# Optimization experiments

Hardware: AMD Instinct MI355X
Metric: run time of the kernel (lower is better)

Reference implementation:

```python
import jax, jax.numpy as jnp
import numpy as np


def _l2norm(x, eps=1e-12):
    # F.normalize(p=2, dim=-1): x / max(||x||_2, eps)
    n = jnp.linalg.norm(x, axis=-1, keepdims=True)
    return x / jnp.maximum(n, eps)


def _dwconv3x3(x, w):
    # depthwise 3x3 conv, padding=1, no bias. x: [B,C,H,W], w: [C,1,3,3]
    return jax.lax.conv_general_dilated(
        x, w, window_strides=(1, 1), padding='SAME',
        feature_group_count=x.shape[1],
        dimension_numbers=('NCHW', 'OIHW', 'NCHW'))


def setup_inputs() -> dict:
    key = jax.random.key(0)
    ks = jax.random.split(key, 10)
    B, H, W, C = 2, 256, 256, 64
    heads, dh, dim_out = 8, 64, 64
    hd = heads * dh  # 512
    s = 0.02
    return {
        'x_in': jax.random.normal(ks[0], (B, H, W, C), jnp.float32),
        'Wq': jax.random.normal(ks[1], (C, hd), jnp.float32) * s,
        'Wk': jax.random.normal(ks[2], (C, hd), jnp.float32) * s,
        'Wv': jax.random.normal(ks[3], (C, hd), jnp.float32) * s,
        'rescale': jnp.ones((heads, 1, 1), jnp.float32),
        'Wproj': jax.random.normal(ks[4], (hd, dim_out), jnp.float32) * s,
        'bproj': jnp.zeros((dim_out,), jnp.float32),
        'Wc1d': jax.random.normal(ks[5], (hd, dim_out), jnp.float32) * s,
        'bc1d': jnp.zeros((dim_out,), jnp.float32),
        'Wpe1': jax.random.normal(ks[6], (dim_out, 1, 3, 3), jnp.float32) * s,
        'Wpe2': jax.random.normal(ks[7], (dim_out, 1, 3, 3), jnp.float32) * s,
    }


def reference(x_in, Wq, Wk, Wv, rescale, Wproj, bproj, Wc1d, bc1d, Wpe1, Wpe2):
    b, h, w, c = x_in.shape
    heads = rescale.shape[0]
    hd = Wq.shape[1]
    dh = hd // heads
    dim_out = Wproj.shape[1]
    ds = 2

    # AvgPool2d(2,2) on channels-last input
    xp = x_in.reshape(b, h // ds, ds, w // ds, ds, c).mean(axis=(2, 4))
    n_ds = (h // ds) * (w // ds)
    xd = xp.reshape(b, n_ds, c)

    # q,k from downsampled tokens; v from full-res tokens
    q = (xd @ Wq).reshape(b, n_ds, heads, dh).transpose(0, 2, 3, 1)   # [b,heads,dh,n_ds]
    k = (xd @ Wk).reshape(b, n_ds, heads, dh).transpose(0, 2, 3, 1)   # [b,heads,dh,n_ds]
    v_inp = x_in.reshape(b, h * w, c) @ Wv                             # [b,n,hd]
    v = v_inp.reshape(b, h * w, heads, dh).transpose(0, 2, 3, 1)       # [b,heads,dh,n]

    q = _l2norm(q)
    k = _l2norm(k)

    # channel (transposed) attention: [b,heads,dh,dh]
    attn = jnp.einsum('bhin,bhjn->bhij', k, q) * rescale
    attn = jax.nn.softmax(attn, axis=-1)

    xa = jnp.einsum('bhij,bhjn->bhin', attn, v)                        # [b,heads,dh,n]
    xa = xa.transpose(0, 3, 1, 2).reshape(b, h * w, hd)                # [b,n,hd]
    out_c = (xa @ Wproj + bproj).reshape(b, h, w, dim_out)

    # positional branch: 1x1 conv (pointwise) then two depthwise 3x3 convs with GELU
    p = v_inp @ Wc1d + bc1d                                            # [b,n,dim_out]
    p = p.reshape(b, h, w, dim_out).transpose(0, 3, 1, 2)              # [b,dim_out,h,w]
    p = _dwconv3x3(p, Wpe1)
    p = jax.nn.gelu(p, approximate=False)
    p = _dwconv3x3(p, Wpe2)
    out_p = p.transpose(0, 2, 3, 1)                                    # [b,h,w,dim_out]

    return out_c + out_p
```

## Files before the change

kernel.cpp:

```cpp
#include <hip/hip_runtime.h>
#include <math.h>


typedef unsigned short u16;
typedef unsigned int u32;
typedef __attribute__((ext_vector_type(8))) short short8;
typedef __attribute__((ext_vector_type(4))) float f32x4;

__device__ __forceinline__ float bf2f(u16 h) { return __uint_as_float(((u32)h) << 16); }
__device__ __forceinline__ u16 f2bf(float f) {
    u32 u = __float_as_uint(f);
    return (u16)((u + 0x7fffu + ((u >> 16) & 1u)) >> 16);
}
__device__ __forceinline__ float rbf(float f) { return bf2f(f2bf(f)); }
__device__ __forceinline__ u32 pk2(float lo, float hi) {
    return (u32)f2bf(lo) | ((u32)f2bf(hi) << 16);
}
__device__ __forceinline__ void unpack8(uint4 v, float* f) {
    u32 a[4] = {v.x, v.y, v.z, v.w};
#pragma unroll
    for (int i = 0; i < 4; ++i) {
        f[2 * i]     = __uint_as_float(a[i] << 16);
        f[2 * i + 1] = __uint_as_float(a[i] & 0xffff0000u);
    }
}
__device__ __forceinline__ float gelu_exact(float v) {
    return 0.5f * v * (1.f + erff(v * 0.70710678118654752f));
}

__global__ __launch_bounds__(256) void k_front(
    const float* __restrict__ x,
    const float* __restrict__ wq_f, const float* __restrict__ wk_f,
    const float* __restrict__ wv_f, const float* __restrict__ rs_f,
    const float* __restrict__ wp_f, const float* __restrict__ bp_f,
    const float* __restrict__ wc_f, const float* __restrict__ bc_f,
    const float* __restrict__ p1_f, const float* __restrict__ p2_f,
    u32* __restrict__ wb32, float* __restrict__ Wpos,
    u16* __restrict__ xb, float* __restrict__ partials) {
    __shared__ float xvs[64 * 68];
    int blk = blockIdx.x;
    int t = threadIdx.x;
    if (blk < 323) {
        u32 pid = (u32)blk * 256u + t;
        if (pid < 82564u) {
            const float* src; u32 p;
            if      (pid < 16384u) { src = wq_f; p = pid; }
            else if (pid < 32768u) { src = wk_f; p = pid - 16384u; }
            else if (pid < 49152u) { src = wv_f; p = pid - 32768u; }
            else if (pid < 49156u) { src = rs_f; p = pid - 49152u; }
            else if (pid < 65540u) { src = wp_f; p = pid - 49156u; }
            else if (pid < 65572u) { src = bp_f; p = pid - 65540u; }
            else if (pid < 81956u) { src = wc_f; p = pid - 65572u; }
            else if (pid < 81988u) { src = bc_f; p = pid - 81956u; }
            else if (pid < 82276u) { src = p1_f; p = pid - 81988u; }
            else                   { src = p2_f; p = pid - 82276u; }
            wb32[pid] = (u32)f2bf(src[2 * p]) | ((u32)f2bf(src[2 * p + 1]) << 16);
        }
    } else if (blk < 387) {
        int c = blk - 323;
        int o = t & 63, ch = t >> 6;
        const float* wvr = wv_f + c * 512 + ch * 128;
        const float* wcr = wc_f + (size_t)(ch * 128) * 64 + o;
        float s = 0.f;
        for (int kk = 0; kk < 128; ++kk)
            s += rbf(wvr[kk]) * rbf(wcr[(size_t)kk * 64]);
        xvs[ch * 64 + o] = s;
        __syncthreads();
        if (t < 64)
            Wpos[c * 64 + t] = (xvs[t] + xvs[64 + t]) + (xvs[128 + t] + xvs[192 + t]);
    } else {
        int gb = blk - 387;
        int b = gb >> 8, sub = gb & 255;
        int py = sub >> 1, half = sub & 1;
        const size_t rowbase = (size_t)(b * 256 + 2 * py) * 16384 + (size_t)half * 8192;
#pragma unroll
        for (int i2 = 0; i2 < 4; ++i2) {
            int u = t + 256 * i2;
            int P = u >> 4, cq = u & 15;
            size_t o0 = rowbase + (size_t)(2 * P) * 64 + cq * 4;
            float4 a0 = *(const float4*)(x + o0);
            float4 a1 = *(const float4*)(x + o0 + 64);
            float4 a2 = *(const float4*)(x + o0 + 16384);
            float4 a3 = *(const float4*)(x + o0 + 16384 + 64);
            *(uint2*)(xb + o0)              = make_uint2(pk2(a0.x, a0.y), pk2(a0.z, a0.w));
            *(uint2*)(xb + o0 + 64)         = make_uint2(pk2(a1.x, a1.y), pk2(a1.z, a1.w));
            *(uint2*)(xb + o0 + 16384)      = make_uint2(pk2(a2.x, a2.y), pk2(a2.z, a2.w));
            *(uint2*)(xb + o0 + 16384 + 64) = make_uint2(pk2(a3.x, a3.y), pk2(a3.z, a3.w));
            float4 s;
            s.x = 0.25f * (a0.x + a1.x + a2.x + a3.x);
            s.y = 0.25f * (a0.y + a1.y + a2.y + a3.y);
            s.z = 0.25f * (a0.z + a1.z + a2.z + a3.z);
            s.w = 0.25f * (a0.w + a1.w + a2.w + a3.w);
            *(float4*)(&xvs[P * 68 + cq * 4]) = s;
        }
        __syncthreads();
        int r0 = (t >> 4) << 2, c0 = (t & 15) << 2;
        float acc[4][4] = {{0.f}};
        for (int P = 0; P < 64; ++P) {
            float4 av = *(const float4*)(&xvs[P * 68 + r0]);
            float4 bv = *(const float4*)(&xvs[P * 68 + c0]);
            float ar[4] = {av.x, av.y, av.z, av.w};
            float br[4] = {bv.x, bv.y, bv.z, bv.w};
#pragma unroll
            for (int i = 0; i < 4; ++i)
#pragma unroll
                for (int j = 0; j < 4; ++j)
                    acc[i][j] += ar[i] * br[j];
        }
        float* outp = partials + (size_t)gb * 4096;
#pragma unroll
        for (int i = 0; i < 4; ++i)
            *(float4*)(&outp[(r0 + i) * 64 + c0]) =
                make_float4(acc[i][0], acc[i][1], acc[i][2], acc[i][3]);
    }
}

__global__ __launch_bounds__(256) void k_mid1(
    const float* __restrict__ partials, float* __restrict__ G4, float* __restrict__ Weff,
    const u16* __restrict__ xb, const float* __restrict__ Wpos,
    const u16* __restrict__ bc1d, u16* __restrict__ pbuf) {
    __shared__ u16 sm[128 * 72];
    int blk = blockIdx.x;
    int t = threadIdx.x;
    if (blk < 128) {
        int gid = blk * 256 + t;
        int e = gid & 4095, ch = (gid >> 12) & 3, b = gid >> 14;
        const float* p0 = partials + ((size_t)(b * 256 + ch * 64)) * 4096 + e;
        float s = 0.f;
        for (int p = 0; p < 64; ++p)
            s += p0[(size_t)p * 4096];
        G4[gid] = s;
        if (gid < 8192) Weff[gid] = 0.f;
        return;
    }
    int pb = blk - 128;
    int lane = t & 63, wv = t >> 6;
    int col = lane & 15, quad = lane >> 4;

    short8 bf[2][4];
#pragma unroll
    for (int kh = 0; kh < 2; ++kh)
#pragma unroll
        for (int nt = 0; nt < 4; ++nt) {
            short8 v;
#pragma unroll
            for (int j = 0; j < 8; ++j)
                v[j] = (short)f2bf(Wpos[(kh * 32 + quad * 8 + j) * 64 + nt * 16 + col]);
            bf[kh][nt] = v;
        }
    float bias[4];
#pragma unroll
    for (int nt = 0; nt < 4; ++nt) bias[nt] = bf2f(bc1d[nt * 16 + col]);

    size_t base = (size_t)pb * 128;
#pragma unroll
    for (int g = 0; g < 2; ++g) {
        int P0 = wv * 32 + g * 16;
        const short8* ap = (const short8*)(xb + (base + P0 + col) * 64);
        short8 a0 = ap[quad];
        short8 a1 = ap[4 + quad];
#pragma unroll
        for (int nt = 0; nt < 4; ++nt) {
            f32x4 acc = {0.f, 0.f, 0.f, 0.f};
            acc = __builtin_amdgcn_mfma_f32_16x16x32_bf16(a0, bf[0][nt], acc, 0, 0, 0);
            acc = __builtin_amdgcn_mfma_f32_16x16x32_bf16(a1, bf[1][nt], acc, 0, 0, 0);
#pragma unroll
            for (int r = 0; r < 4; ++r)
                sm[(P0 + quad * 4 + r) * 72 + nt * 16 + col] = f2bf(acc[r] + bias[nt]);
        }
    }
    __syncthreads();
#pragma unroll
    for (int k = 0; k < 4; ++k) {
        int linear = k * 256 + t;
        int px = linear >> 3, oct = linear & 7;
        uint4 v = *(const uint4*)(&sm[px * 72 + oct * 8]);
        *(uint4*)(pbuf + (base + px) * 64 + oct * 8) = v;
    }
}

__global__ __launch_bounds__(256) void k_mid2(
    const u16* __restrict__ wkb, const u16* __restrict__ wqb,
    const u16* __restrict__ wpb, const u16* __restrict__ wvb,
    const u16* __restrict__ rsb,
    const float* __restrict__ G4, float* __restrict__ Weff,
    const u16* __restrict__ pbuf, const u16* __restrict__ wpe1, u16* __restrict__ tbuf) {
    __shared__ __align__(16) char shm[53248];
    int blk = blockIdx.x, t = threadIdx.x;
    if (blk < 16) {
        float* Ts   = (float*)shm;
        float* Ps   = (float*)(shm + 17408);
        float* Gs   = (float*)(shm + 34816);
        u16*   Wpjs = (u16*)(shm + 34816);
        u16*   Wvs  = (u16*)(shm + 34816 + 9216);
        float* attns = Ps;
        float* Pls   = Ts;
        int b = blk >> 3, h = blk & 7;
        int c = t >> 2, jq = t & 3, j0 = jq * 16;
        {
            int base = t * 16;
            int row = base >> 6, col = base & 63;
            const float* Gb = G4 + (size_t)b * 16384;
#pragma unroll
            for (int q = 0; q < 4; ++q) {
                float4 g0 = *(const float4*)(&Gb[base + 4 * q]);
                float4 g1 = *(const float4*)(&Gb[4096 + base + 4 * q]);
                float4 g2 = *(const float4*)(&Gb[8192 + base + 4 * q]);
                float4 g3 = *(const float4*)(&Gb[12288 + base + 4 * q]);
                *(float4*)(&Gs[row * 68 + col + 4 * q]) = make_float4(
                    (g0.x + g1.x) + (g2.x + g3.x), (g0.y + g1.y) + (g2.y + g3.y),
                    (g0.z + g1.z) + (g2.z + g3.z), (g0.w + g1.w) + (g2.w + g3.w));
            }
        }
        __syncthreads();
        float Tr[16];
        {
#pragma unroll
            for (int jj = 0; jj < 16; ++jj) Tr[jj] = 0.f;
            for (int k = 0; k < 64; ++k) {
                short8 w0 = *(const short8*)(&wkb[k * 512 + h * 64 + j0]);
                short8 w1 = *(const short8*)(&wkb[k * 512 + h * 64 + j0 + 8]);
                float g = Gs[c * 68 + k];
#pragma unroll
                for (int jj = 0; jj < 8; ++jj) {
                    Tr[jj]     += g * bf2f((u16)w0[jj]);
                    Tr[8 + jj] += g * bf2f((u16)w1[jj]);
                }
            }
            short8 wc0 = *(const short8*)(&wkb[c * 512 + h * 64 + j0]);
            short8 wc1 = *(const short8*)(&wkb[c * 512 + h * 64 + j0 + 8]);
#pragma unroll
            for (int jj = 0; jj < 8; ++jj) {
                Ps[c * 68 + j0 + jj]     = bf2f((u16)wc0[jj]) * Tr[jj];
                Ps[c * 68 + j0 + 8 + jj] = bf2f((u16)wc1[jj]) * Tr[8 + jj];
            }
        }
        __syncthreads();
        if (t < 64) {
            float s = 0.f;
            for (int cc = 0; cc < 64; ++cc) s += Ps[cc * 68 + t];
            Ts[t * 68 + 64] = fmaxf(sqrtf(fmaxf(s, 0.f)), 1e-12f);
        }
        {
#pragma unroll
            for (int jj = 0; jj < 16; ++jj) Tr[jj] = 0.f;
            for (int k = 0; k < 64; ++k) {
                short8 w0 = *(const short8*)(&wqb[k * 512 + h * 64 + j0]);
                short8 w1 = *(const short8*)(&wqb[k * 512 + h * 64 + j0 + 8]);
                float g = Gs[c * 68 + k];
#pragma unroll
                for (int jj = 0; jj < 8; ++jj) {
                    Tr[jj]     += g * bf2f((u16)w0[jj]);
                    Tr[8 + jj] += g * bf2f((u16)w1[jj]);
                }
            }
#pragma unroll
            for (int q = 0; q < 4; ++q)
                *(float4*)(&Ts[c * 68 + j0 + 4 * q]) =
                    make_float4(Tr[4 * q], Tr[4 * q + 1], Tr[4 * q + 2], Tr[4 * q + 3]);
        }
        __syncthreads();
        {
            short8 wc0 = *(const short8*)(&wqb[c * 512 + h * 64 + j0]);
            short8 wc1 = *(const short8*)(&wqb[c * 512 + h * 64 + j0 + 8]);
#pragma unroll
            for (int jj = 0; jj < 8; ++jj) {
                Ps[c * 68 + j0 + jj]     = bf2f((u16)wc0[jj]) * Tr[jj];
                Ps[c * 68 + j0 + 8 + jj] = bf2f((u16)wc1[jj]) * Tr[8 + jj];
            }
            *(short8*)(&Wpjs[c * 72 + j0])     = *(const short8*)(&wpb[(h * 64 + c) * 64 + j0]);
            *(short8*)(&Wpjs[c * 72 + j0 + 8]) = *(const short8*)(&wpb[(h * 64 + c) * 64 + j0 + 8]);
        }
        __syncthreads();
        if (t < 64) {
            float s = 0.f;
            for (int cc = 0; cc < 64; ++cc) s += Ps[cc * 68 + t];
            Ts[t * 68 + 65] = fmaxf(sqrtf(fmaxf(s, 0.f)), 1e-12f);
        }
        __syncthreads();
        {
            int i = t >> 2;
            float L[16];
#pragma unroll
            for (int jj = 0; jj < 16; ++jj) L[jj] = 0.f;
            for (int c2 = 0; c2 < 64; ++c2) {
                float wk = bf2f(wkb[c2 * 512 + h * 64 + i]);
#pragma unroll
                for (int q = 0; q < 4; ++q) {
                    float4 tv = *(const float4*)(&Ts[c2 * 68 + j0 + 4 * q]);
                    L[4 * q + 0] += wk * tv.x;
                    L[4 * q + 1] += wk * tv.y;
                    L[4 * q + 2] += wk * tv.z;
                    L[4 * q + 3] += wk * tv.w;
                }
            }
            float rs = bf2f(rsb[h]);
            float nki = Ts[i * 68 + 64];
            float nqv[16];
#pragma unroll
            for (int jj = 0; jj < 16; ++jj) nqv[jj] = Ts[(j0 + jj) * 68 + 65];
            float m = -1e30f;
#pragma unroll
            for (int jj = 0; jj < 16; ++jj) {
                L[jj] = L[jj] * rs / (nki * nqv[jj]);
                m = fmaxf(m, L[jj]);
            }
            m = fmaxf(m, __shfl_xor(m, 1));
            m = fmaxf(m, __shfl_xor(m, 2));
            float s = 0.f;
#pragma unroll
            for (int jj = 0; jj < 16; ++jj) {
                L[jj] = __expf(L[jj] - m);
                s += L[jj];
            }
            s += __shfl_xor(s, 1);
            s += __shfl_xor(s, 2);
            float inv = 1.f / s;
#pragma unroll
            for (int q = 0; q < 4; ++q)
                *(float4*)(&attns[i * 68 + j0 + 4 * q]) =
                    make_float4(L[4 * q] * inv, L[4 * q + 1] * inv,
                                L[4 * q + 2] * inv, L[4 * q + 3] * inv);
        }
        __syncthreads();
        {
            *(short8*)(&Wvs[c * 72 + j0])     = *(const short8*)(&wvb[c * 512 + h * 64 + j0]);
            *(short8*)(&Wvs[c * 72 + j0 + 8]) = *(const short8*)(&wvb[c * 512 + h * 64 + j0 + 8]);
            int j = t >> 2, oq = t & 3;
            float Pl[16];
#pragma unroll
            for (int jj = 0; jj < 16; ++jj) Pl[jj] = 0.f;
            for (int i2 = 0; i2 < 64; ++i2) {
                float a = attns[i2 * 68 + j];
                short8 w0 = *(const short8*)(&Wpjs[i2 * 72 + oq * 16]);
                short8 w1 = *(const short8*)(&Wpjs[i2 * 72 + oq * 16 + 8]);
#pragma unroll
                for (int jj = 0; jj < 8; ++jj) {
                    Pl[jj]     += a * bf2f((u16)w0[jj]);
                    Pl[8 + jj] += a * bf2f((u16)w1[jj]);
                }
            }
#pragma unroll
            for (int q = 0; q < 4; ++q)
                *(float4*)(&Pls[j * 68 + oq * 16 + 4 * q]) =
                    make_float4(Pl[4 * q], Pl[4 * q + 1], Pl[4 * q + 2], Pl[4 * q + 3]);
        }
        __syncthreads();
        {
            int oq = t & 3;
            float acc[16];
#pragma unroll
            for (int jj = 0; jj < 16; ++jj) acc[jj] = 0.f;
            for (int j2 = 0; j2 < 64; ++j2) {
                float wv = bf2f(Wvs[c * 72 + j2]);
#pragma unroll
                for (int q = 0; q < 4; ++q) {
                    float4 pv = *(const float4*)(&Pls[j2 * 68 + oq * 16 + 4 * q]);
                    acc[4 * q + 0] += wv * pv.x;
                    acc[4 * q + 1] += wv * pv.y;
                    acc[4 * q + 2] += wv * pv.z;
                    acc[4 * q + 3] += wv * pv.w;
                }
            }
            float* W = Weff + b * 4096 + c * 64 + oq * 16;
#pragma unroll
            for (int jj = 0; jj < 16; ++jj) atomicAdd(&W[jj], acc[jj]);
        }
        return;
    }
    u16* sm = (u16*)shm;
    int cb = blk - 16;
    int b  = cb >> 9;
    int ty = (cb >> 3) & 63;
    int tx = cb & 7;
    int gy0 = ty * 4, gx0 = tx * 32;

    for (int i = t; i < 1632; i += 256) {
        int px = i >> 3, ch = i & 7;
        int hy = px / 34, hx = px - hy * 34;
        int gy = gy0 + hy - 1, gx = gx0 + hx - 1;
        uint4 v = make_uint4(0, 0, 0, 0);
        if ((unsigned)gy < 256u && (unsigned)gx < 256u)
            v = *(const uint4*)(pbuf + ((size_t)((b << 16) + (gy << 8) + gx)) * 64 + ch * 8);
        *(uint4*)(&sm[px * 72 + ch * 8]) = v;
    }
    int oct = t & 7;
    float w[8][9];
#pragma unroll
    for (int j = 0; j < 8; ++j)
#pragma unroll
        for (int k = 0; k < 9; ++k) w[j][k] = bf2f(wpe1[(oct * 8 + j) * 9 + k]);
    __syncthreads();

#pragma unroll
    for (int s = 0; s < 4; ++s) {
        int lp = (t >> 3) + s * 32;
        int ly = lp >> 5, lx = lp & 31;
        float acc[8] = {0.f, 0.f, 0.f, 0.f, 0.f, 0.f, 0.f, 0.f};
#pragma unroll
        for (int dy = 0; dy < 3; ++dy)
#pragma unroll
            for (int dx = 0; dx < 3; ++dx) {
                int hp = (ly + dy) * 34 + lx + dx;
                uint4 v = *(const uint4*)(&sm[hp * 72 + oct * 8]);
                float f[8];
                unpack8(v, f);
                int tap = dy * 3 + dx;
#pragma unroll
                for (int j = 0; j < 8; ++j) acc[j] += f[j] * w[j][tap];
            }
        u32 pk[4];
#pragma unroll
        for (int q = 0; q < 4; ++q)
            pk[q] = pk2(gelu_exact(acc[2 * q]), gelu_exact(acc[2 * q + 1]));
        size_t gpix = (size_t)(b << 16) + ((size_t)(gy0 + ly) << 8) + gx0 + lx;
        *(uint4*)(tbuf + gpix * 64 + oct * 8) = make_uint4(pk[0], pk[1], pk[2], pk[3]);
    }
}

__global__ __launch_bounds__(256) void k_final(const u16* __restrict__ xb,
                                               const u16* __restrict__ tbuf,
                                               const float* __restrict__ Weff,
                                               const u16* __restrict__ wpe2,
                                               const u16* __restrict__ bproj,
                                               float* __restrict__ out) {
    __shared__ u16 sm[204 * 72];
    __shared__ float stage[128 * 68];
    int t = threadIdx.x;
    int blk = blockIdx.x;
    int b  = blk >> 9;
    int ty = (blk >> 3) & 63;
    int tx = blk & 7;
    int gy0 = ty * 4, gx0 = tx * 32;

    for (int i = t; i < 1632; i += 256) {
        int px = i >> 3, ch = i & 7;
        int hy = px / 34, hx = px - hy * 34;
        int gy = gy0 + hy - 1, gx = gx0 + hx - 1;
        uint4 v = make_uint4(0, 0, 0, 0);
        if ((unsigned)gy < 256u && (unsigned)gx < 256u)
            v = *(const uint4*)(tbuf + ((size_t)((b << 16) + (gy << 8) + gx)) * 64 + ch * 8);
        *(uint4*)(&sm[px * 72 + ch * 8]) = v;
    }
    int oct = t & 7;
    {
        float w[8][9];
#pragma unroll
        for (int j = 0; j < 8; ++j)
#pragma unroll
            for (int k = 0; k < 9; ++k) w[j][k] = bf2f(wpe2[(oct * 8 + j) * 9 + k]);
        __syncthreads();
#pragma unroll
        for (int s = 0; s < 4; ++s) {
            int lp = (t >> 3) + s * 32;
            int ly = lp >> 5, lx = lp & 31;
            float acc[8] = {0.f, 0.f, 0.f, 0.f, 0.f, 0.f, 0.f, 0.f};
#pragma unroll
            for (int dy = 0; dy < 3; ++dy)
#pragma unroll
                for (int dx = 0; dx < 3; ++dx) {
                    int hp = (ly + dy) * 34 + lx + dx;
                    uint4 v = *(const uint4*)(&sm[hp * 72 + oct * 8]);
                    float f[8];
                    unpack8(v, f);
                    int tap = dy * 3 + dx;
#pragma unroll
                    for (int j = 0; j < 8; ++j) acc[j] += f[j] * w[j][tap];
                }
#pragma unroll
            for (int j = 0; j < 8; ++j)
                stage[lp * 68 + oct * 8 + j] = acc[j];
        }
    }
    __syncthreads();

    int lane = t & 63, wv = t >> 6;
    int col = lane & 15, quad = lane >> 4;
    const float* W = Weff + b * 4096;
    short8 bf[2][4];
#pragma unroll
    for (int kh = 0; kh < 2; ++kh)
#pragma unroll
        for (int nt = 0; nt < 4; ++nt) {
            short8 v;
#pragma unroll
            for (int j = 0; j < 8; ++j)
                v[j] = (short)f2bf(W[(kh * 32 + quad * 8 + j) * 64 + nt * 16 + col]);
            bf[kh][nt] = v;
        }
    float bias[4];
#pragma unroll
    for (int nt = 0; nt < 4; ++nt) bias[nt] = bf2f(bproj[nt * 16 + col]);

#pragma unroll
    for (int g = 0; g < 2; ++g) {
        int grp = wv * 2 + g;
        int ly = grp >> 1;
        int lxb = (grp & 1) * 16;
        size_t rowpix = (size_t)(b << 16) + ((size_t)(gy0 + ly) << 8) + gx0;
        const short8* ap = (const short8*)(xb + (rowpix + lxb + col) * 64);
        short8 a0 = ap[quad];
        short8 a1 = ap[4 + quad];
#pragma unroll
        for (int nt = 0; nt < 4; ++nt) {
            f32x4 acc = {0.f, 0.f, 0.f, 0.f};
            acc = __builtin_amdgcn_mfma_f32_16x16x32_bf16(a0, bf[0][nt], acc, 0, 0, 0);
            acc = __builtin_amdgcn_mfma_f32_16x16x32_bf16(a1, bf[1][nt], acc, 0, 0, 0);
#pragma unroll
            for (int r = 0; r < 4; ++r) {
                int lp = ly * 32 + lxb + quad * 4 + r;
                stage[lp * 68 + nt * 16 + col] += acc[r] + bias[nt];
            }
        }
    }
    __syncthreads();

#pragma unroll
    for (int k = 0; k < 8; ++k) {
        int linear = k * 256 + t;
        int px = linear >> 4, c4 = linear & 15;
        int ly = px >> 5, lx = px & 31;
        float4 v = *(const float4*)(&stage[px * 68 + c4 * 4]);
        size_t gpix = (size_t)(b << 16) + ((size_t)(gy0 + ly) << 8) + gx0 + lx;
        *(float4*)(out + gpix * 64 + c4 * 4) = v;
    }
}

extern "C" void kernel_launch(void* const* d_in, const int* in_sizes, int n_in,
                              void* d_out, int out_size, void* d_ws, size_t ws_size,
                              hipStream_t stream) {
    const float* x = (const float*)d_in[0];
    float* out = (float*)d_out;

    char* w = (char*)d_ws;
    size_t off = 0;
    auto alloc = [&](size_t bytes) -> void* {
        void* p = w + off;
        off += (bytes + 255) & ~(size_t)255;
        return p;
    };
    u16* xb = (u16*)alloc((size_t)16777216 * 2);
    u16* wb = (u16*)alloc((size_t)165128 * 2);
    u16* wqb = wb;
    u16* wkb = wqb + 32768;
    u16* wvb = wkb + 32768;
    u16* rsb = wvb + 32768;
    u16* wpb = rsb + 8;
    u16* bpb = wpb + 32768;
    u16* wcb = bpb + 64;
    u16* bcb = wcb + 32768;
    u16* p1b = bcb + 64;
    u16* p2b = p1b + 576;
    (void)wcb;

    float* partials = (float*)alloc((size_t)512 * 4096 * 4);
    float* G4       = (float*)alloc((size_t)2 * 4 * 4096 * 4);
    float* Weff     = (float*)alloc((size_t)2 * 4096 * 4);
    float* Wpos     = (float*)alloc((size_t)4096 * 4);
    u16*   pbuf     = (u16*)alloc((size_t)2 * 65536 * 64 * 2);
    u16*   tbuf     = (u16*)alloc((size_t)2 * 65536 * 64 * 2);

    hipLaunchKernelGGL(k_front, dim3(899), dim3(256), 0, stream,
                       x,
                       (const float*)d_in[1], (const float*)d_in[2], (const float*)d_in[3],
                       (const float*)d_in[4], (const float*)d_in[5], (const float*)d_in[6],
                       (const float*)d_in[7], (const float*)d_in[8], (const float*)d_in[9],
                       (const float*)d_in[10],
                       (u32*)wb, Wpos, xb, partials);
    hipLaunchKernelGGL(k_mid1, dim3(1152), dim3(256), 0, stream,
                       partials, G4, Weff, xb, Wpos, bcb, pbuf);
    hipLaunchKernelGGL(k_mid2, dim3(1040), dim3(256), 0, stream,
                       wkb, wqb, wpb, wvb, rsb, G4, Weff, pbuf, p1b, tbuf);
    hipLaunchKernelGGL(k_final, dim3(1024), dim3(256), 0, stream,
                       xb, tbuf, Weff, p2b, bpb, out);
}
```

Baseline: 174.0 us.

## Use split-bf16 MFMA for small per-head matrix chains in k_mid2

Replaces the scalar FP32 loops in the 16 head blocks of k_mid2 (G·Wk, G·Wq, the logits, attn·Wproj and Wv·P) with 16x16x32 bf16 MFMA instructions. FP32 operands are split into hi and lo bf16 parts to keep accuracy close to FP32. The logit computation is reordered to reuse the Wk·T product, and the column-sum norms become a four-way parallel reduction through a scratch buffer. This targets the serial latency of these 16 blocks, at the cost of doubled MFMA count and strided scalar global loads of the weight operands.

```diff
diff --git a/kernel.cpp b/kernel.cpp
--- a/kernel.cpp
+++ b/kernel.cpp
@@ -26,6 +26,11 @@
 }
 __device__ __forceinline__ float gelu_exact(float v) {
     return 0.5f * v * (1.f + erff(v * 0.70710678118654752f));
+}
+__device__ __forceinline__ void splitbf(float g, short& hi, short& lo) {
+    u16 hb = f2bf(g);
+    hi = (short)hb;
+    lo = (short)f2bf(g - bf2f(hb));
 }
 
 __global__ __launch_bounds__(256) void k_front(
@@ -188,15 +193,13 @@
     __shared__ __align__(16) char shm[53248];
     int blk = blockIdx.x, t = threadIdx.x;
     if (blk < 16) {
-        float* Ts   = (float*)shm;
-        float* Ps   = (float*)(shm + 17408);
-        float* Gs   = (float*)(shm + 34816);
-        u16*   Wpjs = (u16*)(shm + 34816);
-        u16*   Wvs  = (u16*)(shm + 34816 + 9216);
-        float* attns = Ps;
-        float* Pls   = Ts;
+        float* Ts  = (float*)shm;
+        float* Ps  = (float*)(shm + 17408);
+        float* Gs  = (float*)(shm + 34816);
+        float* scr = (float*)(shm + 52224);
         int b = blk >> 3, h = blk & 7;
-        int c = t >> 2, jq = t & 3, j0 = jq * 16;
+        int lane = t & 63, w = t >> 6;
+        int lr = lane & 15, lq = lane >> 4;
         {
             int base = t * 16;
             int row = base >> 6, col = base & 63;
@@ -213,86 +216,112 @@
             }
         }
         __syncthreads();
-        float Tr[16];
-        {
-#pragma unroll
-            for (int jj = 0; jj < 16; ++jj) Tr[jj] = 0.f;
-            for (int k = 0; k < 64; ++k) {
-                short8 w0 = *(const short8*)(&wkb[k * 512 + h * 64 + j0]);
-                short8 w1 = *(const short8*)(&wkb[k * 512 + h * 64 + j0 + 8]);
-                float g = Gs[c * 68 + k];
+        {
+            short8 ahi[2], alo[2];
+#pragma unroll
+            for (int ks = 0; ks < 2; ++ks) {
+                short8 hi, lo;
 #pragma unroll
                 for (int jj = 0; jj < 8; ++jj) {
-                    Tr[jj]     += g * bf2f((u16)w0[jj]);
-                    Tr[8 + jj] += g * bf2f((u16)w1[jj]);
+                    short h16, l16;
+                    splitbf(Gs[(ks * 32 + lq * 8 + jj) * 68 + w * 16 + lr], h16, l16);
+                    hi[jj] = h16; lo[jj] = l16;
                 }
-            }
-            short8 wc0 = *(const short8*)(&wkb[c * 512 + h * 64 + j0]);
-            short8 wc1 = *(const short8*)(&wkb[c * 512 + h * 64 + j0 + 8]);
-#pragma unroll
-            for (int jj = 0; jj < 8; ++jj) {
-                Ps[c * 68 + j0 + jj]     = bf2f((u16)wc0[jj]) * Tr[jj];
-                Ps[c * 68 + j0 + 8 + jj] = bf2f((u16)wc1[jj]) * Tr[8 + jj];
-            }
+                ahi[ks] = hi; alo[ks] = lo;
+            }
+#pragma unroll
+            for (int sel = 0; sel < 2; ++sel) {
+                const u16* W = sel ? wqb : wkb;
+                float* out = sel ? Ts : Ps;
+#pragma unroll
+                for (int nt = 0; nt < 4; ++nt) {
+                    f32x4 acc = {0.f, 0.f, 0.f, 0.f};
+#pragma unroll
+                    for (int ks = 0; ks < 2; ++ks) {
+                        short8 bv;
+#pragma unroll
+                        for (int jj = 0; jj < 8; ++jj)
+                            bv[jj] = (short)W[(ks * 32 + lq * 8 + jj) * 512 + h * 64 + nt * 16 + lr];
+                        acc = __builtin_amdgcn_mfma_f32_16x16x32_bf16(ahi[ks], bv, acc, 0, 0, 0);
+                        acc = __builtin_amdgcn_mfma_f32_16x16x32_bf16(alo[ks], bv, acc, 0, 0, 0);
+                    }
+#pragma unroll
+                    for (int r = 0; r < 4; ++r)
+                        out[(w * 16 + lq * 4 + r) * 68 + nt * 16 + lr] = acc[r];
+                }
+            }
+        }
+        __syncthreads();
+        {
+            int ci = t & 63, grp = t >> 6;
+            float s = 0.f;
+#pragma unroll
+            for (int cc = 0; cc < 16; ++cc) {
+                int c = grp * 16 + cc;
+                s += bf2f(wkb[c * 512 + h * 64 + ci]) * Ps[c * 68 + ci];
+            }
+            scr[grp * 64 + ci] = s;
         }
         __syncthreads();
         if (t < 64) {
+            float s = (scr[t] + scr[64 + t]) + (scr[128 + t] + scr[192 + t]);
+            Ts[t * 68 + 64] = fmaxf(sqrtf(fmaxf(s, 0.f)), 1e-12f);
+        }
+        {
+            short8 ak[2];
+#pragma unroll
+            for (int ks = 0; ks < 2; ++ks) {
+                short8 v;
+#pragma unroll
+                for (int jj = 0; jj < 8; ++jj)
+                    v[jj] = (short)wkb[(ks * 32 + lq * 8 + jj) * 512 + h * 64 + w * 16 + lr];
+                ak[ks] = v;
+            }
+#pragma unroll
+            for (int nt = 0; nt < 4; ++nt) {
+                f32x4 acc = {0.f, 0.f, 0.f, 0.f};
+#pragma unroll
+                for (int ks = 0; ks < 2; ++ks) {
+                    short8 bhi, blo;
+#pragma unroll
+                    for (int jj = 0; jj < 8; ++jj) {
+                        short h16, l16;
+                        splitbf(Ts[(ks * 32 + lq * 8 + jj) * 68 + nt * 16 + lr], h16, l16);
+                        bhi[jj] = h16; blo[jj] = l16;
+                    }
+                    acc = __builtin_amdgcn_mfma_f32_16x16x32_bf16(ak[ks], bhi, acc, 0, 0, 0);
+                    acc = __builtin_amdgcn_mfma_f32_16x16x32_bf16(ak[ks], blo, acc, 0, 0, 0);
+                }
+#pragma unroll
+                for (int r = 0; r < 4; ++r)
+                    Ps[(w * 16 + lq * 4 + r) * 68 + nt * 16 + lr] = acc[r];
+            }
+        }
+        __syncthreads();
+        {
+            int ci = t & 63, grp = t >> 6;
             float s = 0.f;
-            for (int cc = 0; cc < 64; ++cc) s += Ps[cc * 68 + t];
-            Ts[t * 68 + 64] = fmaxf(sqrtf(fmaxf(s, 0.f)), 1e-12f);
-        }
-        {
-#pragma unroll
-            for (int jj = 0; jj < 16; ++jj) Tr[jj] = 0.f;
-            for (int k = 0; k < 64; ++k) {
-                short8 w0 = *(const short8*)(&wqb[k * 512 + h * 64 + j0]);
-                short8 w1 = *(const short8*)(&wqb[k * 512 + h * 64 + j0 + 8]);
-                float g = Gs[c * 68 + k];
-#pragma unroll
-                for (int jj = 0; jj < 8; ++jj) {
-                    Tr[jj]     += g * bf2f((u16)w0[jj]);
-                    Tr[8 + jj] += g * bf2f((u16)w1[jj]);
-                }
-            }
-#pragma unroll
-            for (int q = 0; q < 4; ++q)
-                *(float4*)(&Ts[c * 68 + j0 + 4 * q]) =
-                    make_float4(Tr[4 * q], Tr[4 * q + 1], Tr[4 * q + 2], Tr[4 * q + 3]);
-        }
-        __syncthreads();
-        {
-            short8 wc0 = *(const short8*)(&wqb[c * 512 + h * 64 + j0]);
-            short8 wc1 = *(const short8*)(&wqb[c * 512 + h * 64 + j0 + 8]);
-#pragma unroll
-            for (int jj = 0; jj < 8; ++jj) {
-                Ps[c * 68 + j0 + jj]     = bf2f((u16)wc0[jj]) * Tr[jj];
-                Ps[c * 68 + j0 + 8 + jj] = bf2f((u16)wc1[jj]) * Tr[8 + jj];
-            }
-            *(short8*)(&Wpjs[c * 72 + j0])     = *(const short8*)(&wpb[(h * 64 + c) * 64 + j0]);
-            *(short8*)(&Wpjs[c * 72 + j0 + 8]) = *(const short8*)(&wpb[(h * 64 + c) * 64 + j0 + 8]);
+#pragma unroll
+            for (int cc = 0; cc < 16; ++cc) {
+                int c = grp * 16 + cc;
+                s += bf2f(wqb[c * 512 + h * 64 + ci]) * Ts[c * 68 + ci];
+            }
+            scr[grp * 64 + ci] = s;
         }
         __syncthreads();
         if (t < 64) {
-            float s = 0.f;
-            for (int cc = 0; cc < 64; ++cc) s += Ps[cc * 68 + t];
+            float s = (scr[t] + scr[64 + t]) + (scr[128 + t] + scr[192 + t]);
             Ts[t * 68 + 65] = fmaxf(sqrtf(fmaxf(s, 0.f)), 1e-12f);
         }
         __syncthreads();
         {
-            int i = t >> 2;
+            int i = t >> 2, jq = t & 3, j0 = jq * 16;
             float L[16];
 #pragma unroll
-            for (int jj = 0; jj < 16; ++jj) L[jj] = 0.f;
-            for (int c2 = 0; c2 < 64; ++c2) {
-                float wk = bf2f(wkb[c2 * 512 + h * 64 + i]);
-#pragma unroll
-                for (int q = 0; q < 4; ++q) {
-                    float4 tv = *(const float4*)(&Ts[c2 * 68 + j0 + 4 * q]);
-                    L[4 * q + 0] += wk * tv.x;
-                    L[4 * q + 1] += wk * tv.y;
-                    L[4 * q + 2] += wk * tv.z;
-                    L[4 * q + 3] += wk * tv.w;
-                }
+            for (int q = 0; q < 4; ++q) {
+                float4 lv = *(const float4*)(&Ps[i * 68 + j0 + 4 * q]);
+                L[4 * q] = lv.x; L[4 * q + 1] = lv.y;
+                L[4 * q + 2] = lv.z; L[4 * q + 3] = lv.w;
             }
             float rs = bf2f(rsb[h]);
             float nki = Ts[i * 68 + 64];
@@ -318,53 +347,67 @@
             float inv = 1.f / s;
 #pragma unroll
             for (int q = 0; q < 4; ++q)
-                *(float4*)(&attns[i * 68 + j0 + 4 * q]) =
+                *(float4*)(&Ps[i * 68 + j0 + 4 * q]) =
                     make_float4(L[4 * q] * inv, L[4 * q + 1] * inv,
                                 L[4 * q + 2] * inv, L[4 * q + 3] * inv);
         }
         __syncthreads();
         {
-            *(short8*)(&Wvs[c * 72 + j0])     = *(const short8*)(&wvb[c * 512 + h * 64 + j0]);
-            *(short8*)(&Wvs[c * 72 + j0 + 8]) = *(const short8*)(&wvb[c * 512 + h * 64 + j0 + 8]);
-            int j = t >> 2, oq = t & 3;
-            float Pl[16];
-#pragma unroll
-            for (int jj = 0; jj < 16; ++jj) Pl[jj] = 0.f;
-            for (int i2 = 0; i2 < 64; ++i2) {
-                float a = attns[i2 * 68 + j];
-                short8 w0 = *(const short8*)(&Wpjs[i2 * 72 + oq * 16]);
-                short8 w1 = *(const short8*)(&Wpjs[i2 * 72 + oq * 16 + 8]);
+            short8 ahi[2], alo[2];
+#pragma unroll
+            for (int ks = 0; ks < 2; ++ks) {
+                short8 hi, lo;
 #pragma unroll
                 for (int jj = 0; jj < 8; ++jj) {
-                    Pl[jj]     += a * bf2f((u16)w0[jj]);
-                    Pl[8 + jj] += a * bf2f((u16)w1[jj]);
+                    short h16, l16;
+                    splitbf(Ps[(ks * 32 + lq * 8 + jj) * 68 + w * 16 + lr], h16, l16);
+                    hi[jj] = h16; lo[jj] = l16;
                 }
-            }
-#pragma unroll
-            for (int q = 0; q < 4; ++q)
-                *(float4*)(&Pls[j * 68 + oq * 16 + 4 * q]) =
-                    make_float4(Pl[4 * q], Pl[4 * q + 1], Pl[4 * q + 2], Pl[4 * q + 3]);
-        }
-        __syncthreads();
-        {
-            int oq = t & 3;
-            float acc[16];
-#pragma unroll
-            for (int jj = 0; jj < 16; ++jj) acc[jj] = 0.f;
-            for (int j2 = 0; j2 < 64; ++j2) {
-                float wv = bf2f(Wvs[c * 72 + j2]);
-#pragma unroll
-                for (int q = 0; q < 4; ++q) {
-                    float4 pv = *(const float4*)(&Pls[j2 * 68 + oq * 16 + 4 * q]);
-                    acc[4 * q + 0] += wv * pv.x;
-                    acc[4 * q + 1] += wv * pv.y;
-                    acc[4 * q + 2] += wv * pv.z;
-                    acc[4 * q + 3] += wv * pv.w;
+                ahi[ks] = hi; alo[ks] = lo;
+            }
+#pragma unroll
+            for (int nt = 0; nt < 4; ++nt) {
+                f32x4 acc = {0.f, 0.f, 0.f, 0.f};
+#pragma unroll
+                for (int ks = 0; ks < 2; ++ks) {
+                    short8 bv;
+#pragma unroll
+                    for (int jj = 0; jj < 8; ++jj)
+                        bv[jj] = (short)wpb[(h * 64 + ks * 32 + lq * 8 + jj) * 64 + nt * 16 + lr];
+                    acc = __builtin_amdgcn_mfma_f32_16x16x32_bf16(ahi[ks], bv, acc, 0, 0, 0);
+                    acc = __builtin_amdgcn_mfma_f32_16x16x32_bf16(alo[ks], bv, acc, 0, 0, 0);
                 }
-            }
-            float* W = Weff + b * 4096 + c * 64 + oq * 16;
-#pragma unroll
-            for (int jj = 0; jj < 16; ++jj) atomicAdd(&W[jj], acc[jj]);
+#pragma unroll
+                for (int r = 0; r < 4; ++r)
+                    Ts[(w * 16 + lq * 4 + r) * 68 + nt * 16 + lr] = acc[r];
+            }
+        }
+        __syncthreads();
+        {
+            short8 av[2];
+#pragma unroll
+            for (int ks = 0; ks < 2; ++ks)
+                av[ks] = *(const short8*)(&wvb[(w * 16 + lr) * 512 + h * 64 + ks * 32 + lq * 8]);
+            float* W = Weff + b * 4096;
+#pragma unroll
+            for (int nt = 0; nt < 4; ++nt) {
+                f32x4 acc = {0.f, 0.f, 0.f, 0.f};
+#pragma unroll
+                for (int ks = 0; ks < 2; ++ks) {
+                    short8 bhi, blo;
+#pragma unroll
+                    for (int jj = 0; jj < 8; ++jj) {
+                        short h16, l16;
+                        splitbf(Ts[(ks * 32 + lq * 8 + jj) * 68 + nt * 16 + lr], h16, l16);
+                        bhi[jj] = h16; blo[jj] = l16;
+                    }
+                    acc = __builtin_amdgcn_mfma_f32_16x16x32_bf16(av[ks], bhi, acc, 0, 0, 0);
+                    acc = __builtin_amdgcn_mfma_f32_16x16x32_bf16(av[ks], blo, acc, 0, 0, 0);
+                }
+#pragma unroll
+                for (int r = 0; r < 4; ++r)
+                    atomicAdd(&W[(w * 16 + lq * 4 + r) * 64 + nt * 16 + lr], acc[r]);
+            }
         }
         return;
     }
```

Result: faster. 156.5 us (-10.1%).
